# Kernel optimization log

Measured on AMD Instinct MI355X. Metric: run time of the kernel, lower is better.

Reference implementation:

```python
import jax, jax.numpy as jnp
import numpy as np
import math

M = 0.5
S = 64.0
COS_M = math.cos(M)
SIN_M = math.sin(M)
MIN_COS = math.cos(math.pi - M)
NUM_CLASSES = 100000


def _l2norm(x, eps=1e-12):
    # matches F.normalize: x / max(||x||, eps)
    n = jnp.sqrt(jnp.sum(x * x, axis=-1, keepdims=True))
    return x / jnp.maximum(n, eps)


def setup_inputs() -> dict:
    key = jax.random.key(0)
    k1, k2, k3 = jax.random.split(key, 3)
    feats = jax.random.normal(k1, (8, 128, 512), dtype=jnp.float32)
    w = jax.random.normal(k2, (NUM_CLASSES, 512), dtype=jnp.float32)
    labels = jax.random.randint(k3, (1024,), 0, NUM_CLASSES, dtype=jnp.int32)
    return {"feats": feats, "w": w, "labels": labels}


def reference(feats, w, labels):
    d = feats.shape[-1]
    f = _l2norm(feats).reshape(-1, d)          # [N, d]
    wn = _l2norm(w)                            # [C, d]
    cos_theta = jnp.clip(jnp.einsum('nd,cd->nc', f, wn), -1.0, 1.0)  # [N, C]
    sin_theta = jnp.sqrt(1.0 - cos_theta * cos_theta + 1e-5)
    cos_theta_m = cos_theta * COS_M - sin_theta * SIN_M
    target_logit = jnp.where(cos_theta > MIN_COS, cos_theta_m,
                             cos_theta - sin_theta * M)
    # apply margin only at the label column
    onehot = jax.nn.one_hot(labels, cos_theta.shape[1], dtype=cos_theta.dtype)
    logits = (onehot * target_logit + (1.0 - onehot) * cos_theta) * S
    logp = jax.nn.log_softmax(logits, axis=-1)
    nll = -jnp.take_along_axis(logp, labels[:, None].astype(jnp.int32), axis=1)[:, 0]
    return jnp.mean(nll)
```

## Files before the change

kernel.cpp:

```cpp
#include <hip/hip_runtime.h>
#include <hip/hip_bf16.h>
#include <stdint.h>

#define NUM_CLASSES 100000
#define C_PAD       100096
#define NROWS       1024
#define KDIM        512
#define BM          128
#define BN          128
#define BK          32
#define NKT         (KDIM / BK)
#define TILE_BYTES  8192
#define RB_BYTES    (NKT * TILE_BYTES)
#define RB_U16      (RB_BYTES / 2)

#define L2E64 92.3324826f

typedef __bf16 bf16x8 __attribute__((ext_vector_type(8)));
typedef float  f32x4  __attribute__((ext_vector_type(4)));
typedef unsigned short u16x8 __attribute__((ext_vector_type(8)));

__device__ __forceinline__ unsigned short f2bf(float x) {
    unsigned int u = __float_as_uint(x);
    u = u + 0x7fffu + ((u >> 16) & 1u);
    return (unsigned short)(u >> 16);
}
__device__ __forceinline__ float bf2f(unsigned short x) {
    return __uint_as_float(((unsigned int)x) << 16);
}
__device__ __forceinline__ float fexp64(float c) {
    return exp2f(fmaf(c, L2E64, -L2E64));
}
__device__ __forceinline__ void gload_lds16(const void* g, void* l) {
    __builtin_amdgcn_global_load_lds(
        (const __attribute__((address_space(1))) unsigned int*)g,
        (__attribute__((address_space(3))) unsigned int*)l,
        16, 0, 0);
}


__global__ void norm_rows_tiled(const float* __restrict__ in,
                                unsigned short* __restrict__ out,
                                int rows_valid) {
    __shared__ __align__(16) unsigned short stg[4 * 64 * 8];
    const int tid  = threadIdx.x;
    const int lane = tid & 63;
    const int wv   = tid >> 6;
    const int row  = blockIdx.x * 4 + wv;

    u16x8 o;
    #pragma unroll
    for (int i = 0; i < 8; ++i) o[i] = 0;
    if (row < rows_valid) {
        const float4* p = (const float4*)(in + (size_t)row * KDIM + lane * 8);
        float4 a = p[0], b = p[1];
        float ss = a.x*a.x + a.y*a.y + a.z*a.z + a.w*a.w
                 + b.x*b.x + b.y*b.y + b.z*b.z + b.w*b.w;
        #pragma unroll
        for (int m = 1; m < 64; m <<= 1) ss += __shfl_xor(ss, m, 64);
        float scale = 1.0f / fmaxf(sqrtf(ss), 1e-12f);
        float v[8] = {a.x, a.y, a.z, a.w, b.x, b.y, b.z, b.w};
        #pragma unroll
        for (int i = 0; i < 8; ++i) o[i] = f2bf(v[i] * scale);
    }
    *(u16x8*)&stg[(wv * 64 + lane) * 8] = o;
    __syncthreads();

    const int c    = tid >> 2;
    const int r4   = tid & 3;
    const int rowg = blockIdx.x * 4 + r4;
    u16x8 v = *(const u16x8*)&stg[(r4 * 64 + c) * 8];
    const size_t dst = (size_t)(rowg >> 7) * RB_U16
                     + (c >> 2) * 4096 + (c & 3) * 1024 + (rowg & 127) * 8;
    *(u16x8*)(out + dst) = v;
}

__global__ __launch_bounds__(256) void arcface_gemm(
        const unsigned short* __restrict__ fbT,
        const unsigned short* __restrict__ wbT,
        float* __restrict__ rowsum) {
    __shared__ __align__(16) unsigned short ldsA[2][BM * BK];
    __shared__ __align__(16) unsigned short ldsB[2][BN * BK];
    __shared__ float lds_rs[BM];

    const int tid  = threadIdx.x;
    const int lane = tid & 63;
    const int wid  = tid >> 6;
    const int wr   = wid >> 1;
    const int wc   = wid & 1;
    const int l15  = lane & 15;
    const int kg   = lane >> 4;

    const int wgid = (blockIdx.x & 7) * 782 + (blockIdx.x >> 3);
    const int colb = wgid >> 3;
    const int mrow = wgid & 7;
    const int row0 = mrow * BM;

    const char* aBase = (const char*)fbT + (size_t)mrow * RB_BYTES;
    const char* bBase = (const char*)wbT + (size_t)colb * RB_BYTES;

    f32x4 acc[4][4];
    #pragma unroll
    for (int m = 0; m < 4; ++m)
        #pragma unroll
        for (int n = 0; n < 4; ++n)
            #pragma unroll
            for (int j = 0; j < 4; ++j) acc[m][n][j] = 0.f;

    const int o0 = tid * 16;

    #pragma unroll
    for (int ch = 0; ch < 2; ++ch) {
        const int o = o0 + ch * 4096;
        gload_lds16(aBase + o, (char*)ldsA[0] + o);
        gload_lds16(bBase + o, (char*)ldsB[0] + o);
    }
    __syncthreads();

    int cur = 0;
    for (int kt = 0; kt < NKT; ++kt) {
        if (kt + 1 < NKT) {
            const char* aT = aBase + (kt + 1) * TILE_BYTES;
            const char* bT = bBase + (kt + 1) * TILE_BYTES;
            #pragma unroll
            for (int ch = 0; ch < 2; ++ch) {
                const int o = o0 + ch * 4096;
                gload_lds16(aT + o, (char*)ldsA[cur ^ 1] + o);
                gload_lds16(bT + o, (char*)ldsB[cur ^ 1] + o);
            }
        }

        bf16x8 af[4], bfr[4];
        #pragma unroll
        for (int m = 0; m < 4; ++m) {
            const int rr = wr * 64 + m * 16 + l15;
            af[m] = *(const bf16x8*)((const char*)ldsA[cur] + kg * 2048 + rr * 16);
        }
        #pragma unroll
        for (int n = 0; n < 4; ++n) {
            const int cr = wc * 64 + n * 16 + l15;
            bfr[n] = *(const bf16x8*)((const char*)ldsB[cur] + kg * 2048 + cr * 16);
        }
        #pragma unroll
        for (int m = 0; m < 4; ++m)
            #pragma unroll
            for (int n = 0; n < 4; ++n)
                acc[m][n] = __builtin_amdgcn_mfma_f32_16x16x32_bf16(
                                af[m], bfr[n], acc[m][n], 0, 0, 0);

        __syncthreads();
        cur ^= 1;
    }

    if (tid < BM) lds_rs[tid] = 0.f;
    __syncthreads();

    float rs[4][4];
    #pragma unroll
    for (int m = 0; m < 4; ++m)
        #pragma unroll
        for (int j = 0; j < 4; ++j) rs[m][j] = 0.f;

    #pragma unroll
    for (int n = 0; n < 4; ++n) {
        #pragma unroll
        for (int m = 0; m < 4; ++m) {
            #pragma unroll
            for (int j = 0; j < 4; ++j) {
                float c = acc[m][n][j];
                c = fminf(fmaxf(c, -1.f), 1.f);
                rs[m][j] += fexp64(c);
            }
        }
    }
    #pragma unroll
    for (int m = 0; m < 4; ++m) {
        #pragma unroll
        for (int j = 0; j < 4; ++j) {
            float v = rs[m][j];
            v += __shfl_xor(v, 1, 64);
            v += __shfl_xor(v, 2, 64);
            v += __shfl_xor(v, 4, 64);
            v += __shfl_xor(v, 8, 64);
            rs[m][j] = v;
        }
    }
    if (l15 == 0) {
        #pragma unroll
        for (int m = 0; m < 4; ++m)
            #pragma unroll
            for (int j = 0; j < 4; ++j)
                atomicAdd(&lds_rs[wr * 64 + m * 16 + kg * 4 + j], rs[m][j]);
    }
    __syncthreads();
    if (tid < BM) atomicAdd(&rowsum[row0 + tid], lds_rs[tid]);
}

__global__ void label_dot(const unsigned short* __restrict__ fbT,
                          const unsigned short* __restrict__ wbT,
                          const int* __restrict__ labels,
                          float* __restrict__ coslab) {
    const int lane = threadIdx.x & 63;
    const int row  = blockIdx.x * 4 + (threadIdx.x >> 6);
    if (row >= NROWS) return;
    const int lab = labels[row];
    const size_t fo = (size_t)(row >> 7) * RB_U16 + (lane >> 2) * 4096
                    + (lane & 3) * 1024 + (row & 127) * 8;
    const size_t wo = (size_t)(lab >> 7) * RB_U16 + (lane >> 2) * 4096
                    + (lane & 3) * 1024 + (lab & 127) * 8;
    u16x8 a = *(const u16x8*)(fbT + fo);
    u16x8 b = *(const u16x8*)(wbT + wo);
    float s = 0.f;
    #pragma unroll
    for (int i = 0; i < 8; ++i) s = fmaf(bf2f(a[i]), bf2f(b[i]), s);
    #pragma unroll
    for (int m = 1; m < 64; m <<= 1) s += __shfl_xor(s, m, 64);
    if (lane == 0) coslab[row] = s;
}

__global__ void finalize(const float* __restrict__ rowsum,
                         const float* __restrict__ coslab,
                         float* __restrict__ out) {
    const float COS_M   =  0.87758256189f;
    const float SIN_M   =  0.47942553860f;
    const float MIN_COS = -0.87758256189f;
    __shared__ float red[256];
    const int tid = threadIdx.x;
    float acc = 0.f;
    for (int r = tid; r < NROWS; r += 256) {
        float c = fminf(fmaxf(coslab[r], -1.f), 1.f);
        float sn = sqrtf(1.f - c * c + 1e-5f);
        float cm = c * COS_M - sn * SIN_M;
        float target = (c > MIN_COS) ? cm : (c - sn * 0.5f);
        float adj = rowsum[r] - fexp64(c) + fexp64(target);
        acc += 64.f + logf(adj) - 64.f * target;
    }
    red[tid] = acc;
    __syncthreads();
    for (int s = 128; s > 0; s >>= 1) {
        if (tid < s) red[tid] += red[tid + s];
        __syncthreads();
    }
    if (tid == 0) out[0] = red[0] / (float)NROWS;
}

extern "C" void kernel_launch(void* const* d_in, const int* in_sizes, int n_in,
                              void* d_out, int out_size, void* d_ws, size_t ws_size,
                              hipStream_t stream) {
    const float* feats  = (const float*)d_in[0];
    const float* w      = (const float*)d_in[1];
    const int*   labels = (const int*)d_in[2];
    float* out = (float*)d_out;

    char* ws = (char*)d_ws;
    unsigned short* wbT = (unsigned short*)ws;
    unsigned short* fbT = (unsigned short*)(ws + (size_t)C_PAD * KDIM * 2);
    float* rowsum = (float*)(ws + (size_t)C_PAD * KDIM * 2
                                + (size_t)NROWS * KDIM * 2);
    float* coslab = rowsum + NROWS;

    hipMemsetAsync(rowsum, 0, NROWS * sizeof(float), stream);
    norm_rows_tiled<<<C_PAD / 4, 256, 0, stream>>>(w, wbT, NUM_CLASSES);
    norm_rows_tiled<<<NROWS / 4, 256, 0, stream>>>(feats, fbT, NROWS);
    arcface_gemm<<<(C_PAD / BN) * (NROWS / BM), 256, 0, stream>>>(fbT, wbT, rowsum);
    label_dot<<<NROWS / 4, 256, 0, stream>>>(fbT, wbT, labels, coslab);
    finalize<<<1, 256, 0, stream>>>(rowsum, coslab, out);
}
```

Baseline: 465.4 us.

## Make GEMM persistent with LDS-resident A strip and direct-global B fragments

The GEMM becomes a persistent kernel of 512 blocks. Each block keeps a full 64-row by 512-K strip of normalized features in LDS and loops over column chunks of 256 classes. Each wave reads its B fragments straight from global memory into registers instead of staging them through double-buffered LDS, which removes all per-k-tile barriers. Row sums stay in registers across chunks and are written with per-wave global atomics, so the LDS reduction is gone. The risk is exposed global-load latency on B with no software prefetch, and only 64-row tiles, which lowers MFMA arithmetic intensity per B byte.

```diff
diff --git a/kernel.cpp b/kernel.cpp
--- a/kernel.cpp
+++ b/kernel.cpp
@@ -4,12 +4,10 @@
 
 #define NUM_CLASSES 100000
 #define C_PAD       100096
+#define NCHUNK      391
 #define NROWS       1024
 #define KDIM        512
-#define BM          128
-#define BN          128
-#define BK          32
-#define NKT         (KDIM / BK)
+#define NKT         16
 #define TILE_BYTES  8192
 #define RB_BYTES    (NKT * TILE_BYTES)
 #define RB_U16      (RB_BYTES / 2)
@@ -75,125 +73,101 @@
     *(u16x8*)(out + dst) = v;
 }
 
-__global__ __launch_bounds__(256) void arcface_gemm(
+__global__ __launch_bounds__(256, 2) void arcface_gemm(
         const unsigned short* __restrict__ fbT,
         const unsigned short* __restrict__ wbT,
         float* __restrict__ rowsum) {
-    __shared__ __align__(16) unsigned short ldsA[2][BM * BK];
-    __shared__ __align__(16) unsigned short ldsB[2][BN * BK];
-    __shared__ float lds_rs[BM];
+    __shared__ __align__(16) unsigned short ldsA[32768];
 
     const int tid  = threadIdx.x;
     const int lane = tid & 63;
     const int wid  = tid >> 6;
-    const int wr   = wid >> 1;
-    const int wc   = wid & 1;
     const int l15  = lane & 15;
     const int kg   = lane >> 4;
 
-    const int wgid = (blockIdx.x & 7) * 782 + (blockIdx.x >> 3);
-    const int colb = wgid >> 3;
-    const int mrow = wgid & 7;
-    const int row0 = mrow * BM;
-
-    const char* aBase = (const char*)fbT + (size_t)mrow * RB_BYTES;
-    const char* bBase = (const char*)wbT + (size_t)colb * RB_BYTES;
-
-    f32x4 acc[4][4];
+    const int swz  = (blockIdx.x & 7) * 64 + (blockIdx.x >> 3);
+    const int mblk = swz & 15;
+    const int g    = swz >> 4;
+    const int row0 = mblk * 64;
+
+    const char* aBase = (const char*)fbT + (size_t)(mblk >> 1) * RB_BYTES;
+    const int   roffB = (mblk & 1) * (64 * 16);
+    const char* wbB   = (const char*)wbT;
+
+    #pragma unroll
+    for (int i = 0; i < 16; ++i) {
+        const int c  = i * 256 + tid;
+        const int kt = c >> 8;
+        const int kr = c & 255;
+        gload_lds16(aBase + kt * 8192 + (kr >> 6) * 2048 + roffB + (kr & 63) * 16,
+                    (char*)ldsA + c * 16);
+    }
+    __syncthreads();
+
+    float rsAcc[4][4];
     #pragma unroll
     for (int m = 0; m < 4; ++m)
         #pragma unroll
-        for (int n = 0; n < 4; ++n)
-            #pragma unroll
-            for (int j = 0; j < 4; ++j) acc[m][n][j] = 0.f;
-
-    const int o0 = tid * 16;
-
-    #pragma unroll
-    for (int ch = 0; ch < 2; ++ch) {
-        const int o = o0 + ch * 4096;
-        gload_lds16(aBase + o, (char*)ldsA[0] + o);
-        gload_lds16(bBase + o, (char*)ldsB[0] + o);
-    }
-    __syncthreads();
-
-    int cur = 0;
-    for (int kt = 0; kt < NKT; ++kt) {
-        if (kt + 1 < NKT) {
-            const char* aT = aBase + (kt + 1) * TILE_BYTES;
-            const char* bT = bBase + (kt + 1) * TILE_BYTES;
-            #pragma unroll
-            for (int ch = 0; ch < 2; ++ch) {
-                const int o = o0 + ch * 4096;
-                gload_lds16(aT + o, (char*)ldsA[cur ^ 1] + o);
-                gload_lds16(bT + o, (char*)ldsB[cur ^ 1] + o);
-            }
+        for (int j = 0; j < 4; ++j) rsAcc[m][j] = 0.f;
+
+    for (int jc = 0; jc < 13; ++jc) {
+        const int cchunk = g + 32 * jc;
+        if (cchunk >= NCHUNK) break;
+        const int col0 = cchunk * 256 + wid * 64;
+        const char* bBase = wbB + (size_t)(col0 >> 7) * RB_BYTES
+                                + (col0 & 127) * 16;
+
+        f32x4 acc[4][4];
+        #pragma unroll
+        for (int m = 0; m < 4; ++m)
+            #pragma unroll
+            for (int n = 0; n < 4; ++n)
+                #pragma unroll
+                for (int j = 0; j < 4; ++j) acc[m][n][j] = 0.f;
+
+        for (int kt = 0; kt < NKT; ++kt) {
+            bf16x8 bfr[4], af[4];
+            #pragma unroll
+            for (int n = 0; n < 4; ++n)
+                bfr[n] = *(const bf16x8*)(bBase + kt * 8192 + kg * 2048
+                                          + (n * 16 + l15) * 16);
+            #pragma unroll
+            for (int m = 0; m < 4; ++m)
+                af[m] = *(const bf16x8*)((const char*)ldsA + kt * 4096 + kg * 1024
+                                         + (m * 16 + l15) * 16);
+            #pragma unroll
+            for (int m = 0; m < 4; ++m)
+                #pragma unroll
+                for (int n = 0; n < 4; ++n)
+                    acc[m][n] = __builtin_amdgcn_mfma_f32_16x16x32_bf16(
+                                    af[m], bfr[n], acc[m][n], 0, 0, 0);
         }
 
-        bf16x8 af[4], bfr[4];
-        #pragma unroll
-        for (int m = 0; m < 4; ++m) {
-            const int rr = wr * 64 + m * 16 + l15;
-            af[m] = *(const bf16x8*)((const char*)ldsA[cur] + kg * 2048 + rr * 16);
-        }
-        #pragma unroll
-        for (int n = 0; n < 4; ++n) {
-            const int cr = wc * 64 + n * 16 + l15;
-            bfr[n] = *(const bf16x8*)((const char*)ldsB[cur] + kg * 2048 + cr * 16);
-        }
         #pragma unroll
         for (int m = 0; m < 4; ++m)
             #pragma unroll
             for (int n = 0; n < 4; ++n)
-                acc[m][n] = __builtin_amdgcn_mfma_f32_16x16x32_bf16(
-                                af[m], bfr[n], acc[m][n], 0, 0, 0);
-
-        __syncthreads();
-        cur ^= 1;
-    }
-
-    if (tid < BM) lds_rs[tid] = 0.f;
-    __syncthreads();
-
-    float rs[4][4];
-    #pragma unroll
-    for (int m = 0; m < 4; ++m)
-        #pragma unroll
-        for (int j = 0; j < 4; ++j) rs[m][j] = 0.f;
-
-    #pragma unroll
-    for (int n = 0; n < 4; ++n) {
-        #pragma unroll
-        for (int m = 0; m < 4; ++m) {
-            #pragma unroll
-            for (int j = 0; j < 4; ++j) {
-                float c = acc[m][n][j];
-                c = fminf(fmaxf(c, -1.f), 1.f);
-                rs[m][j] += fexp64(c);
-            }
-        }
-    }
+                #pragma unroll
+                for (int j = 0; j < 4; ++j) {
+                    float c = acc[m][n][j];
+                    c = fminf(fmaxf(c, -1.f), 1.f);
+                    rsAcc[m][j] += fexp64(c);
+                }
+    }
+
     #pragma unroll
     for (int m = 0; m < 4; ++m) {
         #pragma unroll
         for (int j = 0; j < 4; ++j) {
-            float v = rs[m][j];
+            float v = rsAcc[m][j];
             v += __shfl_xor(v, 1, 64);
             v += __shfl_xor(v, 2, 64);
             v += __shfl_xor(v, 4, 64);
             v += __shfl_xor(v, 8, 64);
-            rs[m][j] = v;
+            if (l15 == 0)
+                atomicAdd(&rowsum[row0 + m * 16 + kg * 4 + j], v);
         }
     }
-    if (l15 == 0) {
-        #pragma unroll
-        for (int m = 0; m < 4; ++m)
-            #pragma unroll
-            for (int j = 0; j < 4; ++j)
-                atomicAdd(&lds_rs[wr * 64 + m * 16 + kg * 4 + j], rs[m][j]);
-    }
-    __syncthreads();
-    if (tid < BM) atomicAdd(&rowsum[row0 + tid], lds_rs[tid]);
 }
 
 __global__ void label_dot(const unsigned short* __restrict__ fbT,
@@ -262,7 +236,7 @@
     hipMemsetAsync(rowsum, 0, NROWS * sizeof(float), stream);
     norm_rows_tiled<<<C_PAD / 4, 256, 0, stream>>>(w, wbT, NUM_CLASSES);
     norm_rows_tiled<<<NROWS / 4, 256, 0, stream>>>(feats, fbT, NROWS);
-    arcface_gemm<<<(C_PAD / BN) * (NROWS / BM), 256, 0, stream>>>(fbT, wbT, rowsum);
+    arcface_gemm<<<512, 256, 0, stream>>>(fbT, wbT, rowsum);
     label_dot<<<NROWS / 4, 256, 0, stream>>>(fbT, wbT, labels, coslab);
     finalize<<<1, 256, 0, stream>>>(rowsum, coslab, out);
 }
```

Measured after the change: 422.7 us. 9.2% less time.
